# Kernel tuning notes

Measured on AMD Instinct MI355X. Metric: run time of the kernel, lower is better.

## Reference

```python
import jax, jax.numpy as jnp
import numpy as np

B, S, H = 2, 2048, 2048
NH, NKV = 16, 4
HD = H // NH          # 128
N_REP = NH // NKV     # 4


def _rotate_half(x):
    x1, x2 = x[..., : x.shape[-1] // 2], x[..., x.shape[-1] // 2 :]
    return jnp.concatenate((-x2, x1), axis=-1)


def setup_inputs() -> dict:
    key = jax.random.key(0)
    ks = jax.random.split(key, 5)
    hidden_states = jax.random.normal(ks[0], (B, S, H), dtype=jnp.float32)
    # true rotary tables [max_seq_len, head_dim]
    inv_freq = 1.0 / (10000.0 ** (np.arange(0, HD, 2, dtype=np.float32) / HD))
    t = np.arange(S, dtype=np.float32)
    freqs = np.outer(t, inv_freq)                    # [S, HD/2]
    emb = np.concatenate([freqs, freqs], axis=-1)    # [S, HD]
    cos = jnp.asarray(np.cos(emb))
    sin = jnp.asarray(np.sin(emb))
    Wq = jax.random.normal(ks[1], (H, NH * HD), dtype=jnp.float32) * 0.02
    Wk = jax.random.normal(ks[2], (H, NKV * HD), dtype=jnp.float32) * 0.02
    Wv = jax.random.normal(ks[3], (H, NKV * HD), dtype=jnp.float32) * 0.02
    Wo = jax.random.normal(ks[4], (NH * HD, H), dtype=jnp.float32) * 0.02
    attention_mask = jnp.ones((B, S), dtype=jnp.float32)  # 1 = keep
    return {"hidden_states": hidden_states, "cos": cos, "sin": sin,
            "Wq": Wq, "Wk": Wk, "Wv": Wv, "Wo": Wo,
            "attention_mask": attention_mask}


def reference(hidden_states, cos, sin, Wq, Wk, Wv, Wo, attention_mask):
    # Decoder self-attention: is_causal=True, use_rope=True, no cache, eval (dropout off).
    x = hidden_states
    b, s, _ = x.shape
    q = jnp.einsum('bsh,hd->bsd', x, Wq).reshape(b, s, NH, HD).transpose(0, 2, 1, 3)   # [b,nh,s,hd]
    k = jnp.einsum('bsh,hd->bsd', x, Wk).reshape(b, s, NKV, HD)
    v = jnp.einsum('bsh,hd->bsd', x, Wv).reshape(b, s, NKV, HD)
    # GQA repeat_kv: each kv head repeated n_rep times contiguously
    k = jnp.repeat(k, N_REP, axis=2).transpose(0, 2, 1, 3)   # [b,nh,s,hd]
    v = jnp.repeat(v, N_REP, axis=2).transpose(0, 2, 1, 3)
    # RoPE
    c = cos[:s][None, None, :, :]
    sn = sin[:s][None, None, :, :]
    q = q * c + _rotate_half(q) * sn
    k = k * c + _rotate_half(k) * sn
    # attention scores
    scores = jnp.einsum('bhqd,bhkd->bhqk', q, k) / jnp.sqrt(jnp.float32(HD))
    neg_inf = jnp.finfo(scores.dtype).min
    causal = jnp.triu(jnp.full((s, s), neg_inf, dtype=scores.dtype), k=1)
    scores = scores + causal[None, None, :, :]
    pad = (1.0 - attention_mask[:, None, None, :].astype(scores.dtype)) * neg_inf
    scores = scores + pad
    attn = jax.nn.softmax(scores.astype(jnp.float32), axis=-1).astype(q.dtype)
    out = jnp.einsum('bhqk,bhkd->bhqd', attn, v)             # [b,nh,s,hd]
    out = out.transpose(0, 2, 1, 3).reshape(b, s, NH * HD)
    return jnp.einsum('bsd,dh->bsh', out, Wo)
```

## Files before the change

kernel.cpp:

```cpp
#include <hip/hip_runtime.h>
#include <hip/hip_bf16.h>


typedef __bf16 bf16;
typedef __bf16 bf16x8 __attribute__((ext_vector_type(8)));
typedef __bf16 bf16x4 __attribute__((ext_vector_type(4)));
typedef float  f32x4  __attribute__((ext_vector_type(4)));
typedef float  f32x16 __attribute__((ext_vector_type(16)));

#define MFMA_BF16(a, b, c) __builtin_amdgcn_mfma_f32_16x16x32_bf16((a), (b), (c), 0, 0, 0)
#define MFMA32(a, b, c)    __builtin_amdgcn_mfma_f32_32x32x16_bf16((a), (b), (c), 0, 0, 0)

__device__ __forceinline__ void glds16(const bf16* g, char* l) {
  __builtin_amdgcn_global_load_lds((__attribute__((address_space(1))) const void*)g,
                                   (__attribute__((address_space(3))) void*)l, 16, 0, 0);
}

__global__ __launch_bounds__(256) void k_prep(const float* __restrict__ hs,
                                              bf16* __restrict__ Xbf,
                                              const float* __restrict__ Wq,
                                              const float* __restrict__ Wk,
                                              const float* __restrict__ Wv,
                                              const float* __restrict__ Wo,
                                              bf16* __restrict__ Wtq,
                                              bf16* __restrict__ Wtk,
                                              bf16* __restrict__ Wtv,
                                              bf16* __restrict__ Wto) {
  int blk = blockIdx.x;
  if (blk < 8192) {
    int i = blk * 256 + threadIdx.x;
    float4 v = ((const float4*)hs)[i];
    bf16x4 o;
    o[0] = (bf16)v.x; o[1] = (bf16)v.y; o[2] = (bf16)v.z; o[3] = (bf16)v.w;
    ((bf16x4*)Xbf)[i] = o;
    return;
  }
  int local = blk - 8192;
  const float* W; bf16* Wt; int N;
  if (local < 4096)       { W = Wq; Wt = Wtq; N = 2048; }
  else if (local < 8192)  { W = Wo; Wt = Wto; N = 2048; local -= 4096; }
  else if (local < 9216)  { W = Wk; Wt = Wtk; N = 512;  local -= 8192; }
  else                    { W = Wv; Wt = Wtv; N = 512;  local -= 9216; }
  int kb = (local & 63) * 32, nb = (local >> 6) * 32;
  __shared__ float tile[32][33];
  int tx = threadIdx.x & 31, ty = threadIdx.x >> 5;
#pragma unroll
  for (int i = 0; i < 4; ++i)
    tile[ty + i * 8][tx] = W[(size_t)(kb + ty + i * 8) * N + nb + tx];
  __syncthreads();
#pragma unroll
  for (int i = 0; i < 4; ++i)
    Wt[(size_t)(nb + ty + i * 8) * 2048 + kb + tx] = (bf16)tile[tx][ty + i * 8];
}

__global__ __launch_bounds__(256) void k_rope2(bf16* __restrict__ Qb,
                                               bf16* __restrict__ Kb,
                                               const float* __restrict__ cosb,
                                               const float* __restrict__ sinb,
                                               float sclq) {
  int blk = blockIdx.x;
  bf16* T; int ncols; float scl; int i;
  if (blk < 16384) { T = Qb; ncols = 2048; scl = sclq;  i = blk * 256 + threadIdx.x; }
  else             { T = Kb; ncols = 512;  scl = 1.0f;  i = (blk - 16384) * 256 + threadIdx.x; }
  int npr = ncols >> 1;
  int row = i / npr;
  int p = i - row * npr;
  int h = p >> 6, d = p & 63;
  int c0 = h * 128 + d;
  size_t base = (size_t)row * ncols;
  int s = row & 2047;
  float q0 = (float)T[base + c0];
  float q1 = (float)T[base + c0 + 64];
  float vc0 = cosb[s * 128 + d],      vc1 = cosb[s * 128 + d + 64];
  float vs0 = sinb[s * 128 + d],      vs1 = sinb[s * 128 + d + 64];
  T[base + c0]      = (bf16)((q0 * vc0 - q1 * vs0) * scl);
  T[base + c0 + 64] = (bf16)((q1 * vc1 + q0 * vs1) * scl);
}

__device__ void gemm_n64(const bf16* __restrict__ A, const bf16* __restrict__ Bt,
                         bf16* __restrict__ C, int K, int ldc,
                         int rbase, int cbase, char* sm,
                         bf16* __restrict__ vtr, int vtrow) {
  const int tid = threadIdx.x;
  const int lane = tid & 63, wid = tid >> 6;
  const int l15 = lane & 15, lg = lane >> 4;
  char* Asm = sm;
  char* Bsm = sm + 32768;

  f32x4 acc[2][4];
#pragma unroll
  for (int i = 0; i < 2; ++i)
#pragma unroll
    for (int j = 0; j < 4; ++j)
#pragma unroll
      for (int r = 0; r < 4; ++r) acc[i][j][r] = 0.0f;

  const int ob = wid * 4096 + lane * 16;
  auto stage = [&](int buf, int kb) {
#pragma unroll
    for (int c = 0; c < 4; ++c) {
      int o = ob + c * 1024;
      int r = o >> 7;
      int cc = ((o >> 4) & 7) ^ (r & 7);
      int dst = wid * 4096 + c * 1024 + buf * 16384;
      glds16(A + (size_t)(rbase + r) * K + kb + cc * 8, Asm + dst);
    }
#pragma unroll
    for (int i = 0; i < 2; ++i) {
      int c = wid * 128 + i * 64 + lane;
      int r = c >> 3;
      int cc = (c & 7) ^ (r & 7);
      int dst = wid * 2048 + i * 1024 + buf * 8192;
      glds16(Bt + (size_t)(cbase + r) * K + kb + cc * 8, Bsm + dst);
    }
  };

  stage(0, 0);
  __syncthreads();
  const int nk = K >> 6;
  for (int t = 0; t < nk; ++t) {
    if (t + 1 < nk) stage((t + 1) & 1, (t + 1) << 6);
    const char* At  = Asm + (t & 1) * 16384;
    const char* Bti = Bsm + (t & 1) * 8192;
#pragma unroll
    for (int ks = 0; ks < 2; ++ks) {
      bf16x8 a[2], b[4];
#pragma unroll
      for (int rf = 0; rf < 2; ++rf) {
        int r = wid * 32 + rf * 16 + l15;
        int slot = (ks * 4 + lg) ^ (r & 7);
        a[rf] = *(const bf16x8*)(At + r * 128 + slot * 16);
      }
#pragma unroll
      for (int nf = 0; nf < 4; ++nf) {
        int n = nf * 16 + l15;
        int slot = (ks * 4 + lg) ^ (n & 7);
        b[nf] = *(const bf16x8*)(Bti + n * 128 + slot * 16);
      }
#pragma unroll
      for (int rf = 0; rf < 2; ++rf)
#pragma unroll
        for (int nf = 0; nf < 4; ++nf)
          acc[rf][nf] = MFMA_BF16(a[rf], b[nf], acc[rf][nf]);
    }
    __syncthreads();
  }

  if (vtr != nullptr) {
    __syncthreads();
#pragma unroll
    for (int rf = 0; rf < 2; ++rf)
#pragma unroll
      for (int nf = 0; nf < 4; ++nf) {
        int s0 = wid * 32 + rf * 16 + lg * 4;
        int d = nf * 16 + l15;
        bf16x4 pk;
#pragma unroll
        for (int r = 0; r < 4; ++r) pk[r] = (bf16)acc[rf][nf][r];
        *(bf16x4*)(sm + d * 256 + ((s0 * 2) ^ ((d & 15) << 4))) = pk;
      }
    __syncthreads();
    const int scol = rbase & 2047;
    const int so = tid & 15;
#pragma unroll
    for (int i = 0; i < 4; ++i) {
      int d = (tid >> 4) + i * 16;
      bf16x8 v = *(const bf16x8*)(sm + d * 256 + ((so * 16) ^ ((d & 15) << 4)));
      *(bf16x8*)(vtr + (size_t)(vtrow + d) * 2048 + scol + so * 8) = v;
    }
    return;
  }

#pragma unroll
  for (int rf = 0; rf < 2; ++rf)
#pragma unroll
    for (int nf = 0; nf < 4; ++nf)
#pragma unroll
      for (int r = 0; r < 4; ++r) {
        int row = rbase + wid * 32 + rf * 16 + lg * 4 + r;
        int col = cbase + nf * 16 + l15;
        C[(size_t)row * ldc + col] = (bf16)acc[rf][nf][r];
      }
}

__device__ void gemm_block64(const bf16* __restrict__ A, const bf16* __restrict__ Bt,
                             float* __restrict__ C, int K, int ldc,
                             int rbase, int cbase, char* sm) {
  const int tid = threadIdx.x;
  const int lane = tid & 63, wid = tid >> 6;
  const int l15 = lane & 15, lg = lane >> 4;
  char* Asm = sm;
  char* Bsm = sm + 32768;

  f32x4 acc[2][8];
#pragma unroll
  for (int i = 0; i < 2; ++i)
#pragma unroll
    for (int j = 0; j < 8; ++j)
#pragma unroll
      for (int r = 0; r < 4; ++r) acc[i][j][r] = 0.0f;

  const int ob = wid * 4096 + lane * 16;
  auto stage = [&](int buf, int kb) {
#pragma unroll
    for (int c = 0; c < 4; ++c) {
      int o = ob + c * 1024;
      int r = o >> 7;
      int cc = ((o >> 4) & 7) ^ (r & 7);
      int dst = wid * 4096 + c * 1024 + buf * 16384;
      glds16(A + (size_t)(rbase + r) * K + kb + cc * 8, Asm + dst);
      glds16(Bt + (size_t)(cbase + r) * K + kb + cc * 8, Bsm + dst);
    }
  };

  stage(0, 0);
  __syncthreads();
  const int nk = K >> 6;
  for (int t = 0; t < nk; ++t) {
    if (t + 1 < nk) stage((t + 1) & 1, (t + 1) << 6);
    const char* At  = Asm + (t & 1) * 16384;
    const char* Bti = Bsm + (t & 1) * 16384;
#pragma unroll
    for (int ks = 0; ks < 2; ++ks) {
      bf16x8 a[2], b[8];
#pragma unroll
      for (int rf = 0; rf < 2; ++rf) {
        int r = wid * 32 + rf * 16 + l15;
        int slot = (ks * 4 + lg) ^ (r & 7);
        a[rf] = *(const bf16x8*)(At + r * 128 + slot * 16);
      }
#pragma unroll
      for (int nf = 0; nf < 8; ++nf) {
        int n = nf * 16 + l15;
        int slot = (ks * 4 + lg) ^ (n & 7);
        b[nf] = *(const bf16x8*)(Bti + n * 128 + slot * 16);
      }
#pragma unroll
      for (int rf = 0; rf < 2; ++rf)
#pragma unroll
        for (int nf = 0; nf < 8; ++nf)
          acc[rf][nf] = MFMA_BF16(a[rf], b[nf], acc[rf][nf]);
    }
    __syncthreads();
  }

#pragma unroll
  for (int rf = 0; rf < 2; ++rf)
#pragma unroll
    for (int nf = 0; nf < 8; ++nf)
#pragma unroll
      for (int r = 0; r < 4; ++r) {
        int row = rbase + wid * 32 + rf * 16 + lg * 4 + r;
        int col = cbase + nf * 16 + l15;
        C[(size_t)row * ldc + col] = acc[rf][nf][r];
      }
}

__global__ __launch_bounds__(256, 3) void k_gemm_qkv(const bf16* __restrict__ X,
                                                     const bf16* __restrict__ Wtq,
                                                     const bf16* __restrict__ Wtk,
                                                     const bf16* __restrict__ Wtv,
                                                     bf16* __restrict__ Q,
                                                     bf16* __restrict__ Ko,
                                                     bf16* __restrict__ Vt) {
  __shared__ alignas(16) char sm[49152];
  int nb = blockIdx.y;
  int rbase = blockIdx.x * 128;
  if (nb < 32) {
    gemm_n64(X, Wtq, Q, 2048, 2048, rbase, nb * 64, sm, nullptr, 0);
  } else if (nb < 40) {
    gemm_n64(X, Wtk, Ko, 2048, 512, rbase, (nb - 32) * 64, sm, nullptr, 0);
  } else {
    int vcb = nb - 40;
    int kv = vcb >> 1, d0 = (vcb & 1) * 64;
    int b4 = (rbase >> 11) * 4;
    gemm_n64(X, Wtv, (bf16*)nullptr, 2048, 512, rbase, vcb * 64, sm,
             Vt, (b4 + kv) * 128 + d0);
  }
}

__global__ __launch_bounds__(256, 2) void k_gemm_o(const bf16* __restrict__ AO,
                                                   const bf16* __restrict__ Wto,
                                                   float* __restrict__ Out) {
  __shared__ alignas(16) char sm[65536];
  gemm_block64(AO, Wto, Out, 2048, 2048, blockIdx.x * 128, blockIdx.y * 128, sm);
}

__global__ __launch_bounds__(256, 2) void k_fattn(const bf16* __restrict__ Qg,
                                                  const bf16* __restrict__ Kg,
                                                  const bf16* __restrict__ Vtg,
                                                  bf16* __restrict__ AO) {
  __shared__ alignas(16) char sm[65536];
  const int lane = threadIdx.x & 63, wid = threadIdx.x >> 6;
  const int l31 = lane & 31, lh = lane >> 5;
  const int wg = blockIdx.x;
  const int grp = wg & 7;
  const int b = grp >> 2, kv = grp & 3;
  const int inner = wg >> 3;
  const int head = kv * 4 + (inner & 3);
  const int ih = inner & 31;
  const int strip = (inner < 32) ? (15 - (ih >> 2)) : (ih >> 2);
  const int q0w = strip * 128 + wid * 32;
  const int nt = 2 * (strip + 1);

  const bf16 *ks[4], *vs[4];
#pragma unroll
  for (int i = 0; i < 4; ++i) {
    int c = wid * 256 + i * 64 + lane;
    int kr = c >> 4, kcc = (c & 15) ^ (kr & 15);
    ks[i] = Kg + (size_t)(b * 2048 + kr) * 512 + kv * 128 + kcc * 8;
    int vr = c >> 3, vcc = (c & 7) ^ (vr & 7);
    vs[i] = Vtg + (size_t)((b * 4 + kv) * 128 + vr) * 2048 + vcc * 8;
  }
  auto stage = [&](int t) {
    if (t >= nt) return;
    int kb = t << 6;
    char* base = sm + (t & 1) * 32768 + wid * 4096;
#pragma unroll
    for (int i = 0; i < 4; ++i) {
      glds16(ks[i] + (size_t)kb * 512, base + i * 1024);
      glds16(vs[i] + kb, base + 16384 + i * 1024);
    }
  };

  bf16x8 qf[8];
#pragma unroll
  for (int st = 0; st < 8; ++st)
    qf[st] = *(const bf16x8*)(Qg + (size_t)(b * 2048 + q0w + l31) * 2048 +
                              head * 128 + st * 16 + lh * 8);

  f32x16 o[4];
#pragma unroll
  for (int j = 0; j < 4; ++j)
#pragma unroll
    for (int r = 0; r < 16; ++r) o[j][r] = 0.0f;
  float lrun = 0.0f;
  const float MB = 16.0f;

  stage(0);
  __syncthreads();

  for (int t = 0; t < nt; ++t) {
    const int kb = t << 6;
    stage(t + 1);
    const char* Kt = sm + (t & 1) * 32768;
    const char* Vt = Kt + 16384;

    if (kb <= q0w + 31) {
      f32x16 sa[2];
#pragma unroll
      for (int j = 0; j < 2; ++j)
#pragma unroll
        for (int r = 0; r < 16; ++r) sa[j][r] = 0.0f;
      __builtin_amdgcn_s_setprio(1);
#pragma unroll
      for (int st = 0; st < 8; ++st) {
#pragma unroll
        for (int kt = 0; kt < 2; ++kt) {
          int row = kt * 32 + l31;
          int slot = (st * 2 + lh) ^ (row & 15);
          bf16x8 ka = *(const bf16x8*)(Kt + row * 256 + slot * 16);
          sa[kt] = MFMA32(ka, qf[st], sa[kt]);
        }
      }
      __builtin_amdgcn_s_setprio(0);

      if (kb + 63 > q0w) {
        const int qi = q0w + l31;
#pragma unroll
        for (int kt = 0; kt < 2; ++kt)
#pragma unroll
          for (int r = 0; r < 16; ++r) {
            int kg = kb + kt * 32 + (r & 3) + 8 * (r >> 2) + 4 * lh;
            if (kg > qi) sa[kt][r] = -3e38f;
          }
      }

      union UV { uint32_t u[4]; bf16x8 v; } frag[4];
      float rs = 0.0f;
#pragma unroll
      for (int kt = 0; kt < 2; ++kt) {
        float pe[16];
#pragma unroll
        for (int r = 0; r < 16; ++r) {
          pe[r] = __builtin_amdgcn_exp2f(sa[kt][r] - MB);
          rs += pe[r];
        }
        uint32_t c[8];
#pragma unroll
        for (int g = 0; g < 8; ++g)
          asm("v_cvt_pk_bf16_f32 %0, %1, %2" : "=v"(c[g]) : "v"(pe[2 * g]), "v"(pe[2 * g + 1]));
#pragma unroll
        for (int f = 0; f < 2; ++f) {
          int bi = f * 4;
          uint32_t va = lh ? c[bi + 0] : c[bi + 2];
          uint32_t ra = (uint32_t)__shfl_xor((int)va, 32);
          uint32_t vb = lh ? c[bi + 1] : c[bi + 3];
          uint32_t rb = (uint32_t)__shfl_xor((int)vb, 32);
          UV& fr = frag[kt * 2 + f];
          fr.u[0] = lh ? ra : c[bi + 0];
          fr.u[1] = lh ? rb : c[bi + 1];
          fr.u[2] = lh ? c[bi + 2] : ra;
          fr.u[3] = lh ? c[bi + 3] : rb;
        }
      }
      rs += __shfl_xor(rs, 32);
      lrun += rs;

      __builtin_amdgcn_s_setprio(1);
#pragma unroll
      for (int dt = 0; dt < 4; ++dt) {
        int row = dt * 32 + l31;
#pragma unroll
        for (int kf = 0; kf < 4; ++kf) {
          int slot = (kf * 2 + lh) ^ (row & 7);
          bf16x8 va = *(const bf16x8*)(Vt + row * 128 + slot * 16);
          o[dt] = MFMA32(va, frag[kf].v, o[dt]);
        }
      }
      __builtin_amdgcn_s_setprio(0);
    }
    __syncthreads();
  }

  float linv = 1.0f / lrun;
  bf16* aop = AO + (size_t)(b * 2048 + q0w + l31) * 2048 + head * 128;
#pragma unroll
  for (int dt = 0; dt < 4; ++dt)
#pragma unroll
    for (int g = 0; g < 4; ++g) {
      bf16x4 pk;
#pragma unroll
      for (int j = 0; j < 4; ++j) pk[j] = (bf16)(o[dt][4 * g + j] * linv);
      *(bf16x4*)(aop + dt * 32 + g * 8 + lh * 4) = pk;
    }
}

extern "C" void kernel_launch(void* const* d_in, const int* in_sizes, int n_in,
                              void* d_out, int out_size, void* d_ws, size_t ws_size,
                              hipStream_t stream) {
  const float* hs   = (const float*)d_in[0];
  const float* cosb = (const float*)d_in[1];
  const float* sinb = (const float*)d_in[2];
  const float* Wq   = (const float*)d_in[3];
  const float* Wk   = (const float*)d_in[4];
  const float* Wv   = (const float*)d_in[5];
  const float* Wo   = (const float*)d_in[6];
  float* Out = (float*)d_out;

  char* ws = (char*)d_ws;
  size_t off = 0;
  auto alloc = [&](size_t bytes) { char* p = ws + off; off += bytes; return p; };
  bf16* Xbf = (bf16*)alloc((size_t)4096 * 2048 * 2);
  bf16* Wtq = (bf16*)alloc((size_t)2048 * 2048 * 2);
  bf16* Wtk = (bf16*)alloc((size_t)512 * 2048 * 2);
  bf16* Wtv = (bf16*)alloc((size_t)512 * 2048 * 2);
  bf16* Wto = (bf16*)alloc((size_t)2048 * 2048 * 2);
  bf16* Qb  = (bf16*)alloc((size_t)4096 * 2048 * 2);
  bf16* Kb  = (bf16*)alloc((size_t)4096 * 512 * 2);
  bf16* Vtb = (bf16*)alloc((size_t)4096 * 512 * 2);
  bf16* AO  = (bf16*)alloc((size_t)4096 * 2048 * 2);

  const float SCLQ = 0.08838834764831845f * 1.4426950408889634f;

  k_prep<<<18432, 256, 0, stream>>>(hs, Xbf, Wq, Wk, Wv, Wo, Wtq, Wtk, Wtv, Wto);
  k_gemm_qkv<<<dim3(32, 48), 256, 0, stream>>>(Xbf, Wtq, Wtk, Wtv, Qb, Kb, Vtb);
  k_rope2<<<20480, 256, 0, stream>>>(Qb, Kb, cosb, sinb, SCLQ);
  k_fattn<<<512, 256, 0, stream>>>(Qb, Kb, Vtb, AO);
  k_gemm_o<<<dim3(32, 16), 256, 0, stream>>>(AO, Wto, Out);
}
```

Measured before the change: 187.5 us.

## Split long causal attention strips across two workgroups and combine partials

```diff
diff --git a/kernel.cpp b/kernel.cpp
--- a/kernel.cpp
+++ b/kernel.cpp
@@ -289,7 +289,11 @@
 __global__ __launch_bounds__(256, 2) void k_fattn(const bf16* __restrict__ Qg,
                                                   const bf16* __restrict__ Kg,
                                                   const bf16* __restrict__ Vtg,
-                                                  bf16* __restrict__ AO) {
+                                                  bf16* __restrict__ AO,
+                                                  bf16* __restrict__ PA,
+                                                  bf16* __restrict__ PB,
+                                                  float* __restrict__ LA,
+                                                  float* __restrict__ LB) {
   __shared__ alignas(16) char sm[65536];
   const int lane = threadIdx.x & 63, wid = threadIdx.x >> 6;
   const int l31 = lane & 31, lh = lane >> 5;
@@ -298,10 +302,16 @@
   const int b = grp >> 2, kv = grp & 3;
   const int inner = wg >> 3;
   const int head = kv * 4 + (inner & 3);
-  const int ih = inner & 31;
-  const int strip = (inner < 32) ? (15 - (ih >> 2)) : (ih >> 2);
+  const int idx = inner >> 2;
+  int strip, t0, cnt, half = 0; bool split;
+  if (idx < 16) {
+    strip = 15 - (idx >> 1); half = idx & 1; split = true;
+    cnt = strip + 1; t0 = half * cnt;
+  } else {
+    strip = 23 - idx; split = false;
+    cnt = 2 * (strip + 1); t0 = 0;
+  }
   const int q0w = strip * 128 + wid * 32;
-  const int nt = 2 * (strip + 1);
 
   const bf16 *ks[4], *vs[4];
 #pragma unroll
@@ -312,14 +322,14 @@
     int vr = c >> 3, vcc = (c & 7) ^ (vr & 7);
     vs[i] = Vtg + (size_t)((b * 4 + kv) * 128 + vr) * 2048 + vcc * 8;
   }
-  auto stage = [&](int t) {
-    if (t >= nt) return;
-    int kb = t << 6;
-    char* base = sm + (t & 1) * 32768 + wid * 4096;
-#pragma unroll
-    for (int i = 0; i < 4; ++i) {
-      glds16(ks[i] + (size_t)kb * 512, base + i * 1024);
-      glds16(vs[i] + kb, base + 16384 + i * 1024);
+  auto stage = [&](int i) {
+    if (i >= cnt) return;
+    int kb = (t0 + i) << 6;
+    char* base = sm + (i & 1) * 32768 + wid * 4096;
+#pragma unroll
+    for (int j = 0; j < 4; ++j) {
+      glds16(ks[j] + (size_t)kb * 512, base + j * 1024);
+      glds16(vs[j] + kb, base + 16384 + j * 1024);
     }
   };
 
@@ -340,10 +350,10 @@
   stage(0);
   __syncthreads();
 
-  for (int t = 0; t < nt; ++t) {
-    const int kb = t << 6;
-    stage(t + 1);
-    const char* Kt = sm + (t & 1) * 32768;
+  for (int i = 0; i < cnt; ++i) {
+    const int kb = (t0 + i) << 6;
+    stage(i + 1);
+    const char* Kt = sm + (i & 1) * 32768;
     const char* Vt = Kt + 16384;
 
     if (kb <= q0w + 31) {
@@ -423,17 +433,54 @@
     __syncthreads();
   }
 
-  float linv = 1.0f / lrun;
-  bf16* aop = AO + (size_t)(b * 2048 + q0w + l31) * 2048 + head * 128;
-#pragma unroll
-  for (int dt = 0; dt < 4; ++dt)
-#pragma unroll
-    for (int g = 0; g < 4; ++g) {
-      bf16x4 pk;
-#pragma unroll
-      for (int j = 0; j < 4; ++j) pk[j] = (bf16)(o[dt][4 * g + j] * linv);
-      *(bf16x4*)(aop + dt * 32 + g * 8 + lh * 4) = pk;
-    }
+  if (split) {
+    bf16* pb = half ? PB : PA;
+    size_t prow = (size_t)b * 1024 + (q0w + l31 - 1024);
+    bf16* pop = pb + prow * 2048 + head * 128;
+#pragma unroll
+    for (int dt = 0; dt < 4; ++dt)
+#pragma unroll
+      for (int g = 0; g < 4; ++g) {
+        bf16x4 pk;
+#pragma unroll
+        for (int j = 0; j < 4; ++j) pk[j] = (bf16)o[dt][4 * g + j];
+        *(bf16x4*)(pop + dt * 32 + g * 8 + lh * 4) = pk;
+      }
+    if (lh == 0) (half ? LB : LA)[prow * 16 + head] = lrun;
+  } else {
+    float linv = 1.0f / lrun;
+    bf16* aop = AO + (size_t)(b * 2048 + q0w + l31) * 2048 + head * 128;
+#pragma unroll
+    for (int dt = 0; dt < 4; ++dt)
+#pragma unroll
+      for (int g = 0; g < 4; ++g) {
+        bf16x4 pk;
+#pragma unroll
+        for (int j = 0; j < 4; ++j) pk[j] = (bf16)(o[dt][4 * g + j] * linv);
+        *(bf16x4*)(aop + dt * 32 + g * 8 + lh * 4) = pk;
+      }
+  }
+}
+
+__global__ __launch_bounds__(256) void k_combine(const bf16* __restrict__ PA,
+                                                 const bf16* __restrict__ PB,
+                                                 const float* __restrict__ LA,
+                                                 const float* __restrict__ LB,
+                                                 bf16* __restrict__ AO) {
+  int blk = blockIdx.x;
+  int tid = threadIdx.x;
+  size_t prow = (size_t)blk;
+  int b = blk >> 10;
+  size_t orow = (size_t)b * 2048 + 1024 + (blk & 1023);
+  int col0 = tid * 8;
+  int h = tid >> 4;
+  float inv = 1.0f / (LA[prow * 16 + h] + LB[prow * 16 + h]);
+  bf16x8 a = *(const bf16x8*)(PA + prow * 2048 + col0);
+  bf16x8 c = *(const bf16x8*)(PB + prow * 2048 + col0);
+  bf16x8 o;
+#pragma unroll
+  for (int j = 0; j < 8; ++j) o[j] = (bf16)(((float)a[j] + (float)c[j]) * inv);
+  *(bf16x8*)(AO + orow * 2048 + col0) = o;
 }
 
 extern "C" void kernel_launch(void* const* d_in, const int* in_sizes, int n_in,
@@ -460,12 +507,17 @@
   bf16* Kb  = (bf16*)alloc((size_t)4096 * 512 * 2);
   bf16* Vtb = (bf16*)alloc((size_t)4096 * 512 * 2);
   bf16* AO  = (bf16*)alloc((size_t)4096 * 2048 * 2);
+  bf16* PA  = (bf16*)alloc((size_t)2048 * 2048 * 2);
+  bf16* PB  = (bf16*)alloc((size_t)2048 * 2048 * 2);
+  float* LA = (float*)alloc((size_t)2048 * 16 * 4);
+  float* LB = (float*)alloc((size_t)2048 * 16 * 4);
 
   const float SCLQ = 0.08838834764831845f * 1.4426950408889634f;
 
   k_prep<<<18432, 256, 0, stream>>>(hs, Xbf, Wq, Wk, Wv, Wo, Wtq, Wtk, Wtv, Wto);
   k_gemm_qkv<<<dim3(32, 48), 256, 0, stream>>>(Xbf, Wtq, Wtk, Wtv, Qb, Kb, Vtb);
   k_rope2<<<20480, 256, 0, stream>>>(Qb, Kb, cosb, sinb, SCLQ);
-  k_fattn<<<512, 256, 0, stream>>>(Qb, Kb, Vtb, AO);
+  k_fattn<<<768, 256, 0, stream>>>(Qb, Kb, Vtb, AO, PA, PB, LA, LB);
+  k_combine<<<2048, 256, 0, stream>>>(PA, PB, LA, LB, AO);
   k_gemm_o<<<dim3(32, 16), 256, 0, stream>>>(AO, Wto, Out);
 }
```

New measurement: 193.9 us. 1.03x slower.

## Fuse RoPE into QKV GEMM epilogue via permuted Q/K weight columns

Applied to the files above, without the earlier changes.

```diff
diff --git a/kernel.cpp b/kernel.cpp
--- a/kernel.cpp
+++ b/kernel.cpp
@@ -36,11 +36,11 @@
     return;
   }
   int local = blk - 8192;
-  const float* W; bf16* Wt; int N;
-  if (local < 4096)       { W = Wq; Wt = Wtq; N = 2048; }
-  else if (local < 8192)  { W = Wo; Wt = Wto; N = 2048; local -= 4096; }
-  else if (local < 9216)  { W = Wk; Wt = Wtk; N = 512;  local -= 8192; }
-  else                    { W = Wv; Wt = Wtv; N = 512;  local -= 9216; }
+  const float* W; bf16* Wt; int N; bool perm;
+  if (local < 4096)       { W = Wq; Wt = Wtq; N = 2048; perm = true; }
+  else if (local < 8192)  { W = Wo; Wt = Wto; N = 2048; perm = false; local -= 4096; }
+  else if (local < 9216)  { W = Wk; Wt = Wtk; N = 512;  perm = true;  local -= 8192; }
+  else                    { W = Wv; Wt = Wtv; N = 512;  perm = false; local -= 9216; }
   int kb = (local & 63) * 32, nb = (local >> 6) * 32;
   __shared__ float tile[32][33];
   int tx = threadIdx.x & 31, ty = threadIdx.x >> 5;
@@ -49,37 +49,24 @@
     tile[ty + i * 8][tx] = W[(size_t)(kb + ty + i * 8) * N + nb + tx];
   __syncthreads();
 #pragma unroll
-  for (int i = 0; i < 4; ++i)
-    Wt[(size_t)(nb + ty + i * 8) * 2048 + kb + tx] = (bf16)tile[tx][ty + i * 8];
-}
-
-__global__ __launch_bounds__(256) void k_rope2(bf16* __restrict__ Qb,
-                                               bf16* __restrict__ Kb,
-                                               const float* __restrict__ cosb,
-                                               const float* __restrict__ sinb,
-                                               float sclq) {
-  int blk = blockIdx.x;
-  bf16* T; int ncols; float scl; int i;
-  if (blk < 16384) { T = Qb; ncols = 2048; scl = sclq;  i = blk * 256 + threadIdx.x; }
-  else             { T = Kb; ncols = 512;  scl = 1.0f;  i = (blk - 16384) * 256 + threadIdx.x; }
-  int npr = ncols >> 1;
-  int row = i / npr;
-  int p = i - row * npr;
-  int h = p >> 6, d = p & 63;
-  int c0 = h * 128 + d;
-  size_t base = (size_t)row * ncols;
-  int s = row & 2047;
-  float q0 = (float)T[base + c0];
-  float q1 = (float)T[base + c0 + 64];
-  float vc0 = cosb[s * 128 + d],      vc1 = cosb[s * 128 + d + 64];
-  float vs0 = sinb[s * 128 + d],      vs1 = sinb[s * 128 + d + 64];
-  T[base + c0]      = (bf16)((q0 * vc0 - q1 * vs0) * scl);
-  T[base + c0 + 64] = (bf16)((q1 * vc1 + q0 * vs1) * scl);
+  for (int i = 0; i < 4; ++i) {
+    int n = nb + ty + i * 8;
+    int outn = n;
+    if (perm) {
+      int dl = n & 127;
+      int c = (dl < 64) ? ((dl & 15) | ((dl >> 4) << 5))
+                        : ((dl & 15) | (((dl & 63) >> 4) << 5) | 16);
+      outn = (n & ~127) | c;
+    }
+    Wt[(size_t)outn * 2048 + kb + tx] = (bf16)tile[tx][ty + i * 8];
+  }
 }
 
 __device__ void gemm_n64(const bf16* __restrict__ A, const bf16* __restrict__ Bt,
                          bf16* __restrict__ C, int K, int ldc,
                          int rbase, int cbase, char* sm,
+                         float rope_scl, const float* __restrict__ cosb,
+                         const float* __restrict__ sinb,
                          bf16* __restrict__ vtr, int vtrow) {
   const int tid = threadIdx.x;
   const int lane = tid & 63, wid = tid >> 6;
@@ -144,6 +131,27 @@
           acc[rf][nf] = MFMA_BF16(a[rf], b[nf], acc[rf][nf]);
     }
     __syncthreads();
+  }
+
+  if (rope_scl != 0.0f) {
+    const int half = (cbase >> 6) & 1;
+#pragma unroll
+    for (int rf = 0; rf < 2; ++rf)
+#pragma unroll
+      for (int r = 0; r < 4; ++r) {
+        int s = (rbase + wid * 32 + rf * 16 + lg * 4 + r) & 2047;
+        const float* cb = cosb + s * 128;
+        const float* sb = sinb + s * 128;
+#pragma unroll
+        for (int p = 0; p < 2; ++p) {
+          int d0 = l15 + ((half * 2 + p) << 4);
+          float lo = acc[rf][2 * p][r], hi = acc[rf][2 * p + 1][r];
+          float c0 = cb[d0], c1 = cb[d0 + 64];
+          float s0 = sb[d0], s1 = sb[d0 + 64];
+          acc[rf][2 * p][r]     = (lo * c0 - hi * s0) * rope_scl;
+          acc[rf][2 * p + 1][r] = (hi * c1 + lo * s1) * rope_scl;
+        }
+      }
   }
 
   if (vtr != nullptr) {
@@ -262,20 +270,25 @@
                                                      const bf16* __restrict__ Wtv,
                                                      bf16* __restrict__ Q,
                                                      bf16* __restrict__ Ko,
-                                                     bf16* __restrict__ Vt) {
+                                                     bf16* __restrict__ Vt,
+                                                     const float* __restrict__ cosb,
+                                                     const float* __restrict__ sinb,
+                                                     float sclq) {
   __shared__ alignas(16) char sm[49152];
   int nb = blockIdx.y;
   int rbase = blockIdx.x * 128;
   if (nb < 32) {
-    gemm_n64(X, Wtq, Q, 2048, 2048, rbase, nb * 64, sm, nullptr, 0);
+    gemm_n64(X, Wtq, Q, 2048, 2048, rbase, nb * 64, sm, sclq, cosb, sinb,
+             nullptr, 0);
   } else if (nb < 40) {
-    gemm_n64(X, Wtk, Ko, 2048, 512, rbase, (nb - 32) * 64, sm, nullptr, 0);
+    gemm_n64(X, Wtk, Ko, 2048, 512, rbase, (nb - 32) * 64, sm, 1.0f, cosb, sinb,
+             nullptr, 0);
   } else {
     int vcb = nb - 40;
     int kv = vcb >> 1, d0 = (vcb & 1) * 64;
     int b4 = (rbase >> 11) * 4;
     gemm_n64(X, Wtv, (bf16*)nullptr, 2048, 512, rbase, vcb * 64, sm,
-             Vt, (b4 + kv) * 128 + d0);
+             0.0f, nullptr, nullptr, Vt, (b4 + kv) * 128 + d0);
   }
 }
 
@@ -464,8 +477,8 @@
   const float SCLQ = 0.08838834764831845f * 1.4426950408889634f;
 
   k_prep<<<18432, 256, 0, stream>>>(hs, Xbf, Wq, Wk, Wv, Wo, Wtq, Wtk, Wtv, Wto);
-  k_gemm_qkv<<<dim3(32, 48), 256, 0, stream>>>(Xbf, Wtq, Wtk, Wtv, Qb, Kb, Vtb);
-  k_rope2<<<20480, 256, 0, stream>>>(Qb, Kb, cosb, sinb, SCLQ);
+  k_gemm_qkv<<<dim3(32, 48), 256, 0, stream>>>(Xbf, Wtq, Wtk, Wtv, Qb, Kb, Vtb,
+                                               cosb, sinb, SCLQ);
   k_fattn<<<512, 256, 0, stream>>>(Qb, Kb, Vtb, AO);
   k_gemm_o<<<dim3(32, 16), 256, 0, stream>>>(AO, Wto, Out);
 }
```

New measurement: 179.6 us (median of 3 runs). 1.04x faster.
